# Kernel optimization log

Hardware: AMD Instinct MI355X
Metric: run time of the kernel (lower is better)

The kernel has to match this reference:

```python
import jax, jax.numpy as jnp
import numpy as np

H = 512   # hidden_dim
B = 1024  # batch
D = 256   # history length


def setup_inputs() -> dict:
    key = jax.random.key(0)
    k1, k2, k3, k4, k5, k6 = jax.random.split(key, 6)
    return {
        "h_tilde": jax.random.normal(k1, (B, H), dtype=jnp.float32),
        "c_t": jax.random.normal(k2, (B, H), dtype=jnp.float32),
        "h_history": jax.random.normal(k3, (B, D, H), dtype=jnp.float32),
        # learned parameters (nn.Linear stores weight as [out, in]; y = x @ W.T)
        "Waq": jax.random.normal(k4, (H, 2 * H), dtype=jnp.float32) * (1.0 / np.sqrt(2 * H)),
        "Wah": jax.random.normal(k5, (H, H), dtype=jnp.float32) * (1.0 / np.sqrt(H)),
        "ba": jnp.zeros((H,), dtype=jnp.float32),
        "v_t": jax.random.normal(k6, (H,), dtype=jnp.float32),
    }


def reference(h_tilde, c_t, h_history, Waq, Wah, ba, v_t):
    # q_t = [h_tilde ; c_t] -> [B, 2H]; project to [B, H]
    q_t = jnp.concatenate([h_tilde, c_t], axis=1)
    q_proj = q_t @ Waq.T                         # [B, H]
    h_proj = jnp.einsum('bdh,gh->bdg', h_history, Wah)  # [B, D, H]
    # broadcast add + tanh: the large [B, D, H] intermediate
    score_pre = jnp.tanh(q_proj[:, None, :] + h_proj + ba)
    alpha_unscaled = jnp.einsum('bdh,h->bd', score_pre, v_t)  # [B, D]
    alpha = jax.nn.softmax(alpha_unscaled, axis=1)            # [B, D]
    e_t = jnp.einsum('bd,bdh->bh', alpha, h_history)          # [B, H]
    return (e_t, alpha)
```

## Files before the change

### kernel.cpp

```cpp
#include <hip/hip_runtime.h>
#include <hip/hip_bf16.h>

#define HDIM 512
#define BDIM 1024
#define DDIM 256
#define MTOT (BDIM * DDIM)

typedef _Float16 half8 __attribute__((ext_vector_type(8)));
typedef float f32x4 __attribute__((ext_vector_type(4)));

__device__ __forceinline__ float ftanh(float x) {
    float e = __expf(2.0f * x);
    return 1.0f - 2.0f / (e + 1.0f);
}

__device__ __forceinline__ void gl_lds16(const _Float16* src, _Float16* dst) {
    __builtin_amdgcn_global_load_lds((const __attribute__((address_space(1))) void*)src,
                                     (__attribute__((address_space(3))) void*)dst,
                                     16, 0, 0);
}

__global__ __launch_bounds__(256) void k_convertW(const float* __restrict__ Wah,
                                                  _Float16* __restrict__ W16) {
    int n = blockIdx.x * 256 + threadIdx.x;
    int chunk = n >> 10, r = n & 1023;
    int kb = r >> 6, kp = (r >> 4) & 3, g = r & 15;
    const float* src = Wah + (size_t)(chunk * 16 + g) * 512 + kb * 32 + kp * 8;
    float4 v0 = *(const float4*)src;
    float4 v1 = *(const float4*)(src + 4);
    half8 h;
    h[0] = (_Float16)v0.x; h[1] = (_Float16)v0.y; h[2] = (_Float16)v0.z; h[3] = (_Float16)v0.w;
    h[4] = (_Float16)v1.x; h[5] = (_Float16)v1.y; h[6] = (_Float16)v1.z; h[7] = (_Float16)v1.w;
    *(half8*)&W16[(size_t)n * 8] = h;
}

__global__ __launch_bounds__(256) void k_qproj(const float* __restrict__ h_tilde,
                                               const float* __restrict__ c_t,
                                               const float* __restrict__ Waq,
                                               const float* __restrict__ ba,
                                               float* __restrict__ qb) {
    __shared__ float qs[4][1024];
    int t = threadIdx.x;
    int b0 = blockIdx.x * 4;
    #pragma unroll
    for (int p = 0; p < 4; p++) {
        int f4 = t + p * 256;
        int e = f4 * 4;
        int row = e >> 10, k = e & 1023;
        float4 v;
        if (k < 512) v = *(const float4*)&h_tilde[(b0 + row) * 512 + k];
        else         v = *(const float4*)&c_t[(b0 + row) * 512 + k - 512];
        *(float4*)&qs[row][k] = v;
    }
    __syncthreads();
    int g0 = t, g1 = t + 256;
    float acc0[4] = {0.f, 0.f, 0.f, 0.f};
    float acc1[4] = {0.f, 0.f, 0.f, 0.f};
    const float4* w0p = (const float4*)&Waq[(size_t)g0 * 1024];
    const float4* w1p = (const float4*)&Waq[(size_t)g1 * 1024];
    #pragma unroll 4
    for (int k4 = 0; k4 < 256; k4++) {
        float4 w0 = w0p[k4];
        float4 w1 = w1p[k4];
        #pragma unroll
        for (int bb = 0; bb < 4; bb++) {
            float4 q = *(const float4*)&qs[bb][k4 * 4];
            acc0[bb] += q.x * w0.x + q.y * w0.y + q.z * w0.z + q.w * w0.w;
            acc1[bb] += q.x * w1.x + q.y * w1.y + q.z * w1.z + q.w * w1.w;
        }
    }
    #pragma unroll
    for (int bb = 0; bb < 4; bb++) {
        qb[(b0 + bb) * 512 + g0] = acc0[bb] + ba[g0];
        qb[(b0 + bb) * 512 + g1] = acc1[bb] + ba[g1];
    }
}

__global__ __launch_bounds__(256, 4) void k_logits(const float* __restrict__ hist,
                                                   const float* __restrict__ qb,
                                                   const _Float16* __restrict__ W16,
                                                   const float* __restrict__ v_t,
                                                   float* __restrict__ logits) {
    __shared__ _Float16 Wb[2][8192];
    __shared__ float qbs[512];
    __shared__ float vsh[512];

    int t = threadIdx.x;
    int w = t >> 6, lane = t & 63, l15 = lane & 15, l4 = lane >> 4;
    size_t m_base = (size_t)blockIdx.x * 64;
    int b = blockIdx.x >> 2;

    qbs[t] = qb[b * 512 + t];
    qbs[t + 256] = qb[b * 512 + 256 + t];
    vsh[t] = v_t[t];
    vsh[t + 256] = v_t[256 + t];

    #pragma unroll
    for (int sg = 0; sg < 4; sg++)
        gl_lds16(W16 + ((size_t)(w * 4 + sg) * 64 + lane) * 8,
                 &Wb[0][(w * 4 + sg) * 512]);

    half8 afr[16];
    const float* xb = hist + (m_base + w * 16 + l15) * 512 + l4 * 8;
    #pragma unroll
    for (int kb = 0; kb < 16; kb++) {
        const float* p = xb + kb * 32;
        float4 v0 = *(const float4*)p;
        float4 v1 = *(const float4*)(p + 4);
        half8 h;
        h[0] = (_Float16)v0.x; h[1] = (_Float16)v0.y; h[2] = (_Float16)v0.z; h[3] = (_Float16)v0.w;
        h[4] = (_Float16)v1.x; h[5] = (_Float16)v1.y; h[6] = (_Float16)v1.z; h[7] = (_Float16)v1.w;
        afr[kb] = h;
    }

    float S[4] = {0.f, 0.f, 0.f, 0.f};

    __syncthreads();

    const _Float16* bufbase0 = &Wb[0][lane * 8];
    const _Float16* bufbase1 = &Wb[1][lane * 8];

    for (int c = 0; c < 32; c++) {
        int cur = c & 1;
        if (c < 31) {
            const _Float16* wc = W16 + (size_t)(c + 1) * 8192;
            _Float16* wd = Wb[cur ^ 1];
            #pragma unroll
            for (int sg = 0; sg < 4; sg++)
                gl_lds16(wc + ((size_t)(w * 4 + sg) * 64 + lane) * 8,
                         &wd[(w * 4 + sg) * 512]);
        }
        const _Float16* bufp = cur ? bufbase1 : bufbase0;
        f32x4 tac = (f32x4){0.f, 0.f, 0.f, 0.f};
        __builtin_amdgcn_s_setprio(1);
        #pragma unroll
        for (int kb = 0; kb < 16; kb++) {
            half8 bf = *(const half8*)(bufp + kb * 512);
            tac = __builtin_amdgcn_mfma_f32_16x16x32_f16(afr[kb], bf, tac, 0, 0, 0);
        }
        __builtin_amdgcn_s_setprio(0);
        float qv = qbs[c * 16 + l15];
        float vv = vsh[c * 16 + l15];
        #pragma unroll
        for (int j = 0; j < 4; j++)
            S[j] += ftanh(tac[j] + qv) * vv;
        __syncthreads();
    }

    #pragma unroll
    for (int j = 0; j < 4; j++) {
        float s = S[j];
        s += __shfl_xor(s, 1, 64);
        s += __shfl_xor(s, 2, 64);
        s += __shfl_xor(s, 4, 64);
        s += __shfl_xor(s, 8, 64);
        if (l15 == 0)
            logits[m_base + w * 16 + l4 * 4 + j] = s;
    }
}

__global__ __launch_bounds__(256) void k_softmax_et(const float* __restrict__ hist,
                                                    const float* __restrict__ logits,
                                                    float* __restrict__ out) {
    __shared__ float as_[256];
    __shared__ float wred[4];
    __shared__ float ered[512];
    int b = blockIdx.x, t = threadIdx.x;
    float l = logits[b * 256 + t];
    float m = l;
    m = fmaxf(m, __shfl_xor(m, 1, 64));
    m = fmaxf(m, __shfl_xor(m, 2, 64));
    m = fmaxf(m, __shfl_xor(m, 4, 64));
    m = fmaxf(m, __shfl_xor(m, 8, 64));
    m = fmaxf(m, __shfl_xor(m, 16, 64));
    m = fmaxf(m, __shfl_xor(m, 32, 64));
    if ((t & 63) == 0) wred[t >> 6] = m;
    __syncthreads();
    m = fmaxf(fmaxf(wred[0], wred[1]), fmaxf(wred[2], wred[3]));
    float e = __expf(l - m);
    float s = e;
    s += __shfl_xor(s, 1, 64);
    s += __shfl_xor(s, 2, 64);
    s += __shfl_xor(s, 4, 64);
    s += __shfl_xor(s, 8, 64);
    s += __shfl_xor(s, 16, 64);
    s += __shfl_xor(s, 32, 64);
    __syncthreads();
    if ((t & 63) == 0) wred[t >> 6] = s;
    __syncthreads();
    s = wred[0] + wred[1] + wred[2] + wred[3];
    float a = e / s;
    out[BDIM * HDIM + b * 256 + t] = a;
    as_[t] = a;
    __syncthreads();
    int c4 = (t & 127) * 4;
    int dp = t >> 7;
    float e0 = 0.f, e1 = 0.f, e2 = 0.f, e3 = 0.f;
    const float* hb = hist + (size_t)b * 256 * 512 + c4;
    #pragma unroll 4
    for (int d = dp; d < 256; d += 2) {
        float al = as_[d];
        float4 h = *(const float4*)&hb[(size_t)d * 512];
        e0 += al * h.x; e1 += al * h.y; e2 += al * h.z; e3 += al * h.w;
    }
    if (dp) {
        float4 v; v.x = e0; v.y = e1; v.z = e2; v.w = e3;
        *(float4*)&ered[c4] = v;
    }
    __syncthreads();
    if (!dp) {
        float4 p = *(const float4*)&ered[c4];
        float4 r; r.x = e0 + p.x; r.y = e1 + p.y; r.z = e2 + p.z; r.w = e3 + p.w;
        *(float4*)&out[b * 512 + c4] = r;
    }
}

extern "C" void kernel_launch(void* const* d_in, const int* in_sizes, int n_in,
                              void* d_out, int out_size, void* d_ws, size_t ws_size,
                              hipStream_t stream) {
    const float* h_tilde = (const float*)d_in[0];
    const float* c_t     = (const float*)d_in[1];
    const float* hist    = (const float*)d_in[2];
    const float* Waq     = (const float*)d_in[3];
    const float* Wah     = (const float*)d_in[4];
    const float* ba      = (const float*)d_in[5];
    const float* v_t     = (const float*)d_in[6];
    float* out = (float*)d_out;

    char* ws = (char*)d_ws;
    float*    qb     = (float*)ws;
    _Float16* W16    = (_Float16*)(ws + (2u << 20));
    float*    logits = (float*)(ws + (3u << 20));

    k_convertW<<<128, 256, 0, stream>>>(Wah, W16);
    k_qproj<<<256, 256, 0, stream>>>(h_tilde, c_t, Waq, ba, qb);
    k_logits<<<4096, 256, 0, stream>>>(hist, qb, W16, v_t, logits);
    k_softmax_et<<<1024, 256, 0, stream>>>(hist, logits, out);
}
```

Before: 414.4 us.

## Retile logits GEMM into 128x128 MFMA tiles with fp16 history cache for softmax

Replaces the per-64-row logits kernel with a 128x128 tiled MFMA GEMM that stages both A (history converted to fp16) and B in LDS with double buffering, splitting the N dimension across 4 blocks and writing partial logits. The nb==0 blocks also write an fp16 copy of the history, which the softmax/e_t kernel reads instead of the fp32 tensor, halving that pass's bytes. It merges W conversion and q projection into one prep launch and uses a raw v_rcp in tanh. The cost is 4x reread of the history across N-blocks (likely cache-served), an extra 256MB fp16 write, and reduced precision for e_t.

```diff
diff --git a/kernel.cpp b/kernel.cpp
--- a/kernel.cpp
+++ b/kernel.cpp
@@ -7,11 +7,15 @@
 #define MTOT (BDIM * DDIM)
 
 typedef _Float16 half8 __attribute__((ext_vector_type(8)));
+typedef _Float16 half4_ __attribute__((ext_vector_type(4)));
 typedef float f32x4 __attribute__((ext_vector_type(4)));
 
 __device__ __forceinline__ float ftanh(float x) {
     float e = __expf(2.0f * x);
-    return 1.0f - 2.0f / (e + 1.0f);
+    float d = e + 1.0f;
+    float r;
+    asm("v_rcp_f32 %0, %1" : "=v"(r) : "v"(d));
+    return 1.0f - 2.0f * r;
 }
 
 __device__ __forceinline__ void gl_lds16(const _Float16* src, _Float16* dst) {
@@ -20,153 +24,207 @@
                                      16, 0, 0);
 }
 
-__global__ __launch_bounds__(256) void k_convertW(const float* __restrict__ Wah,
-                                                  _Float16* __restrict__ W16) {
-    int n = blockIdx.x * 256 + threadIdx.x;
-    int chunk = n >> 10, r = n & 1023;
-    int kb = r >> 6, kp = (r >> 4) & 3, g = r & 15;
-    const float* src = Wah + (size_t)(chunk * 16 + g) * 512 + kb * 32 + kp * 8;
-    float4 v0 = *(const float4*)src;
-    float4 v1 = *(const float4*)(src + 4);
-    half8 h;
-    h[0] = (_Float16)v0.x; h[1] = (_Float16)v0.y; h[2] = (_Float16)v0.z; h[3] = (_Float16)v0.w;
-    h[4] = (_Float16)v1.x; h[5] = (_Float16)v1.y; h[6] = (_Float16)v1.z; h[7] = (_Float16)v1.w;
-    *(half8*)&W16[(size_t)n * 8] = h;
-}
-
-__global__ __launch_bounds__(256) void k_qproj(const float* __restrict__ h_tilde,
-                                               const float* __restrict__ c_t,
-                                               const float* __restrict__ Waq,
-                                               const float* __restrict__ ba,
-                                               float* __restrict__ qb) {
-    __shared__ float qs[4][1024];
+__global__ __launch_bounds__(256) void k_prep(const float* __restrict__ h_tilde,
+                                              const float* __restrict__ c_t,
+                                              const float* __restrict__ Waq,
+                                              const float* __restrict__ ba,
+                                              const float* __restrict__ Wah,
+                                              float* __restrict__ qb,
+                                              _Float16* __restrict__ W16) {
+    __shared__ float qs[16][1024];
     int t = threadIdx.x;
-    int b0 = blockIdx.x * 4;
-    #pragma unroll
-    for (int p = 0; p < 4; p++) {
-        int f4 = t + p * 256;
-        int e = f4 * 4;
-        int row = e >> 10, k = e & 1023;
+    if (blockIdx.x >= 256) {
+        int n = (blockIdx.x - 256) * 256 + t;
+        int ch = n >> 9, r = n & 511;
+        int j = r >> 6, l = r & 63;
+        int col = (ch >> 4) * 128 + j * 16 + (l & 15);
+        int k = (ch & 15) * 32 + (l >> 4) * 8;
+        const float* src = Wah + (size_t)col * 512 + k;
+        float4 v0 = *(const float4*)src;
+        float4 v1 = *(const float4*)(src + 4);
+        half8 h;
+        h[0] = (_Float16)v0.x; h[1] = (_Float16)v0.y; h[2] = (_Float16)v0.z; h[3] = (_Float16)v0.w;
+        h[4] = (_Float16)v1.x; h[5] = (_Float16)v1.y; h[6] = (_Float16)v1.z; h[7] = (_Float16)v1.w;
+        *(half8*)&W16[(size_t)n * 8] = h;
+        return;
+    }
+    int bt = blockIdx.x >> 2, gq = blockIdx.x & 3;
+    int b0 = bt * 16;
+    #pragma unroll
+    for (int i = 0; i < 16; i++) {
+        int idx = t + i * 256;
+        int row = idx >> 8, k = (idx & 255) * 4;
         float4 v;
         if (k < 512) v = *(const float4*)&h_tilde[(b0 + row) * 512 + k];
         else         v = *(const float4*)&c_t[(b0 + row) * 512 + k - 512];
         *(float4*)&qs[row][k] = v;
     }
     __syncthreads();
-    int g0 = t, g1 = t + 256;
-    float acc0[4] = {0.f, 0.f, 0.f, 0.f};
-    float acc1[4] = {0.f, 0.f, 0.f, 0.f};
-    const float4* w0p = (const float4*)&Waq[(size_t)g0 * 1024];
-    const float4* w1p = (const float4*)&Waq[(size_t)g1 * 1024];
-    #pragma unroll 4
+    int g = gq * 128 + (t & 127);
+    int bh = t >> 7;
+    float acc[8] = {0.f, 0.f, 0.f, 0.f, 0.f, 0.f, 0.f, 0.f};
+    const float4* wp = (const float4*)&Waq[(size_t)g * 1024];
+    #pragma unroll 2
     for (int k4 = 0; k4 < 256; k4++) {
-        float4 w0 = w0p[k4];
-        float4 w1 = w1p[k4];
-        #pragma unroll
-        for (int bb = 0; bb < 4; bb++) {
-            float4 q = *(const float4*)&qs[bb][k4 * 4];
-            acc0[bb] += q.x * w0.x + q.y * w0.y + q.z * w0.z + q.w * w0.w;
-            acc1[bb] += q.x * w1.x + q.y * w1.y + q.z * w1.z + q.w * w1.w;
-        }
-    }
-    #pragma unroll
-    for (int bb = 0; bb < 4; bb++) {
-        qb[(b0 + bb) * 512 + g0] = acc0[bb] + ba[g0];
-        qb[(b0 + bb) * 512 + g1] = acc1[bb] + ba[g1];
-    }
-}
-
-__global__ __launch_bounds__(256, 4) void k_logits(const float* __restrict__ hist,
-                                                   const float* __restrict__ qb,
-                                                   const _Float16* __restrict__ W16,
-                                                   const float* __restrict__ v_t,
-                                                   float* __restrict__ logits) {
-    __shared__ _Float16 Wb[2][8192];
-    __shared__ float qbs[512];
-    __shared__ float vsh[512];
+        float4 wv = wp[k4];
+        #pragma unroll
+        for (int j = 0; j < 8; j++) {
+            float4 q = *(const float4*)&qs[bh * 8 + j][k4 * 4];
+            acc[j] += q.x * wv.x + q.y * wv.y + q.z * wv.z + q.w * wv.w;
+        }
+    }
+    float bav = ba[g];
+    #pragma unroll
+    for (int j = 0; j < 8; j++)
+        qb[(b0 + bh * 8 + j) * 512 + g] = acc[j] + bav;
+}
+
+template<int STORE16>
+__global__ __launch_bounds__(256, 3) void k_gemm(const float* __restrict__ hist,
+                                                 const float* __restrict__ qb,
+                                                 const _Float16* __restrict__ W16,
+                                                 const float* __restrict__ v_t,
+                                                 float* __restrict__ logitP,
+                                                 _Float16* __restrict__ hist16) {
+    __shared__ _Float16 Ab[2][4096];
+    __shared__ _Float16 Bb[2][4096];
+    __shared__ float qbs[128];
+    __shared__ float vsh[128];
+    __shared__ float red[2][128];
 
     int t = threadIdx.x;
     int w = t >> 6, lane = t & 63, l15 = lane & 15, l4 = lane >> 4;
-    size_t m_base = (size_t)blockIdx.x * 64;
-    int b = blockIdx.x >> 2;
-
-    qbs[t] = qb[b * 512 + t];
-    qbs[t + 256] = qb[b * 512 + 256 + t];
-    vsh[t] = v_t[t];
-    vsh[t + 256] = v_t[256 + t];
-
-    #pragma unroll
-    for (int sg = 0; sg < 4; sg++)
-        gl_lds16(W16 + ((size_t)(w * 4 + sg) * 64 + lane) * 8,
-                 &Wb[0][(w * 4 + sg) * 512]);
-
-    half8 afr[16];
-    const float* xb = hist + (m_base + w * 16 + l15) * 512 + l4 * 8;
-    #pragma unroll
-    for (int kb = 0; kb < 16; kb++) {
-        const float* p = xb + kb * 32;
-        float4 v0 = *(const float4*)p;
-        float4 v1 = *(const float4*)(p + 4);
-        half8 h;
-        h[0] = (_Float16)v0.x; h[1] = (_Float16)v0.y; h[2] = (_Float16)v0.z; h[3] = (_Float16)v0.w;
-        h[4] = (_Float16)v1.x; h[5] = (_Float16)v1.y; h[6] = (_Float16)v1.z; h[7] = (_Float16)v1.w;
-        afr[kb] = h;
-    }
-
-    float S[4] = {0.f, 0.f, 0.f, 0.f};
-
-    __syncthreads();
-
-    const _Float16* bufbase0 = &Wb[0][lane * 8];
-    const _Float16* bufbase1 = &Wb[1][lane * 8];
-
-    for (int c = 0; c < 32; c++) {
-        int cur = c & 1;
-        if (c < 31) {
-            const _Float16* wc = W16 + (size_t)(c + 1) * 8192;
-            _Float16* wd = Wb[cur ^ 1];
+    int bx = blockIdx.x;
+    int xslot = bx & 7, nb = (bx >> 3) & 3;
+    int mt = (bx >> 5) * 8 + xslot;
+    size_t m_base = (size_t)mt * 128;
+    int b = mt >> 1;
+    int wr = w >> 1, wc = w & 1;
+
+    if (t < 128) {
+        qbs[t] = qb[b * 512 + nb * 128 + t];
+        vsh[t] = v_t[nb * 128 + t];
+    }
+
+    const _Float16* wch = W16 + (size_t)nb * 16 * 4096;
+
+    const float* asrc = hist + (m_base + (t >> 1)) * 512 + (t & 1) * 16;
+    const int ga0 = ((t >> 5) * 64 + (t & 1) * 32 + ((t >> 1) & 15)) * 8;
+    const int ga1 = ga0 + 128;
+    _Float16* h16dst = hist16 + (m_base + (t >> 1)) * 512 + (t & 1) * 16;
+
+    #pragma unroll
+    for (int sg = 0; sg < 2; sg++)
+        gl_lds16(wch + ((size_t)(w * 2 + sg) * 64 + lane) * 8,
+                 &Bb[0][(w * 2 + sg) * 512]);
+    float4 xa0 = *(const float4*)(asrc);
+    float4 xa1 = *(const float4*)(asrc + 4);
+    float4 xa2 = *(const float4*)(asrc + 8);
+    float4 xa3 = *(const float4*)(asrc + 12);
+    {
+        half8 h0, h1;
+        h0[0] = (_Float16)xa0.x; h0[1] = (_Float16)xa0.y; h0[2] = (_Float16)xa0.z; h0[3] = (_Float16)xa0.w;
+        h0[4] = (_Float16)xa1.x; h0[5] = (_Float16)xa1.y; h0[6] = (_Float16)xa1.z; h0[7] = (_Float16)xa1.w;
+        h1[0] = (_Float16)xa2.x; h1[1] = (_Float16)xa2.y; h1[2] = (_Float16)xa2.z; h1[3] = (_Float16)xa2.w;
+        h1[4] = (_Float16)xa3.x; h1[5] = (_Float16)xa3.y; h1[6] = (_Float16)xa3.z; h1[7] = (_Float16)xa3.w;
+        *(half8*)&Ab[0][ga0] = h0;
+        *(half8*)&Ab[0][ga1] = h1;
+        if (STORE16 && nb == 0) {
+            *(half8*)(h16dst) = h0;
+            *(half8*)(h16dst + 8) = h1;
+        }
+    }
+    __syncthreads();
+
+    f32x4 acc[4][4];
+    #pragma unroll
+    for (int i = 0; i < 4; i++)
+        #pragma unroll
+        for (int j = 0; j < 4; j++)
+            acc[i][j] = (f32x4){0.f, 0.f, 0.f, 0.f};
+
+    for (int s = 0; s < 16; s++) {
+        int cur = s & 1;
+        if (s < 15) {
+            const _Float16* wc2 = wch + (size_t)(s + 1) * 4096;
+            _Float16* bd = Bb[cur ^ 1];
             #pragma unroll
-            for (int sg = 0; sg < 4; sg++)
-                gl_lds16(wc + ((size_t)(w * 4 + sg) * 64 + lane) * 8,
-                         &wd[(w * 4 + sg) * 512]);
-        }
-        const _Float16* bufp = cur ? bufbase1 : bufbase0;
-        f32x4 tac = (f32x4){0.f, 0.f, 0.f, 0.f};
+            for (int sg = 0; sg < 2; sg++)
+                gl_lds16(wc2 + ((size_t)(w * 2 + sg) * 64 + lane) * 8,
+                         &bd[(w * 2 + sg) * 512]);
+            const float* pa = asrc + (s + 1) * 32;
+            xa0 = *(const float4*)(pa);
+            xa1 = *(const float4*)(pa + 4);
+            xa2 = *(const float4*)(pa + 8);
+            xa3 = *(const float4*)(pa + 12);
+        }
+        const _Float16* ap = Ab[cur];
+        const _Float16* bp = Bb[cur];
+        half8 afv[4], bfv[4];
+        #pragma unroll
+        for (int i = 0; i < 4; i++)
+            afv[i] = *(const half8*)&ap[((wr * 4 + i) * 64 + lane) * 8];
+        #pragma unroll
+        for (int j = 0; j < 4; j++)
+            bfv[j] = *(const half8*)&bp[((wc * 4 + j) * 64 + lane) * 8];
         __builtin_amdgcn_s_setprio(1);
         #pragma unroll
-        for (int kb = 0; kb < 16; kb++) {
-            half8 bf = *(const half8*)(bufp + kb * 512);
-            tac = __builtin_amdgcn_mfma_f32_16x16x32_f16(afr[kb], bf, tac, 0, 0, 0);
-        }
+        for (int i = 0; i < 4; i++)
+            #pragma unroll
+            for (int j = 0; j < 4; j++)
+                acc[i][j] = __builtin_amdgcn_mfma_f32_16x16x32_f16(afv[i], bfv[j], acc[i][j], 0, 0, 0);
         __builtin_amdgcn_s_setprio(0);
-        float qv = qbs[c * 16 + l15];
-        float vv = vsh[c * 16 + l15];
-        #pragma unroll
-        for (int j = 0; j < 4; j++)
-            S[j] += ftanh(tac[j] + qv) * vv;
+        if (s < 15) {
+            half8 h0, h1;
+            h0[0] = (_Float16)xa0.x; h0[1] = (_Float16)xa0.y; h0[2] = (_Float16)xa0.z; h0[3] = (_Float16)xa0.w;
+            h0[4] = (_Float16)xa1.x; h0[5] = (_Float16)xa1.y; h0[6] = (_Float16)xa1.z; h0[7] = (_Float16)xa1.w;
+            h1[0] = (_Float16)xa2.x; h1[1] = (_Float16)xa2.y; h1[2] = (_Float16)xa2.z; h1[3] = (_Float16)xa2.w;
+            h1[4] = (_Float16)xa3.x; h1[5] = (_Float16)xa3.y; h1[6] = (_Float16)xa3.z; h1[7] = (_Float16)xa3.w;
+            _Float16* ad = Ab[cur ^ 1];
+            *(half8*)&ad[ga0] = h0;
+            *(half8*)&ad[ga1] = h1;
+            if (STORE16 && nb == 0) {
+                *(half8*)(h16dst + (s + 1) * 32) = h0;
+                *(half8*)(h16dst + (s + 1) * 32 + 8) = h1;
+            }
+        }
         __syncthreads();
     }
 
     #pragma unroll
-    for (int j = 0; j < 4; j++) {
-        float s = S[j];
-        s += __shfl_xor(s, 1, 64);
-        s += __shfl_xor(s, 2, 64);
-        s += __shfl_xor(s, 4, 64);
-        s += __shfl_xor(s, 8, 64);
-        if (l15 == 0)
-            logits[m_base + w * 16 + l4 * 4 + j] = s;
-    }
-}
-
+    for (int i = 0; i < 4; i++) {
+        #pragma unroll
+        for (int r = 0; r < 4; r++) {
+            float s_ = 0.0f;
+            #pragma unroll
+            for (int j = 0; j < 4; j++) {
+                int col = wc * 64 + j * 16 + l15;
+                s_ += ftanh(acc[i][j][r] + qbs[col]) * vsh[col];
+            }
+            s_ += __shfl_xor(s_, 1, 64);
+            s_ += __shfl_xor(s_, 2, 64);
+            s_ += __shfl_xor(s_, 4, 64);
+            s_ += __shfl_xor(s_, 8, 64);
+            if (l15 == 0)
+                red[wc][wr * 64 + i * 16 + l4 * 4 + r] = s_;
+        }
+    }
+    __syncthreads();
+    if (t < 128)
+        logitP[(size_t)nb * MTOT + m_base + t] = red[0][t] + red[1][t];
+}
+
+template<int USE16>
 __global__ __launch_bounds__(256) void k_softmax_et(const float* __restrict__ hist,
-                                                    const float* __restrict__ logits,
+                                                    const _Float16* __restrict__ h16,
+                                                    const float* __restrict__ logitP,
                                                     float* __restrict__ out) {
     __shared__ float as_[256];
     __shared__ float wred[4];
     __shared__ float ered[512];
     int b = blockIdx.x, t = threadIdx.x;
-    float l = logits[b * 256 + t];
+    int m0i = b * 256 + t;
+    float l = logitP[m0i] + logitP[MTOT + m0i] + logitP[2 * MTOT + m0i] + logitP[3 * MTOT + m0i];
     float m = l;
     m = fmaxf(m, __shfl_xor(m, 1, 64));
     m = fmaxf(m, __shfl_xor(m, 2, 64));
@@ -196,12 +254,23 @@
     int c4 = (t & 127) * 4;
     int dp = t >> 7;
     float e0 = 0.f, e1 = 0.f, e2 = 0.f, e3 = 0.f;
-    const float* hb = hist + (size_t)b * 256 * 512 + c4;
-    #pragma unroll 4
-    for (int d = dp; d < 256; d += 2) {
-        float al = as_[d];
-        float4 h = *(const float4*)&hb[(size_t)d * 512];
-        e0 += al * h.x; e1 += al * h.y; e2 += al * h.z; e3 += al * h.w;
+    if (USE16) {
+        const _Float16* hb = h16 + (size_t)b * 256 * 512 + c4;
+        #pragma unroll 4
+        for (int d = dp; d < 256; d += 2) {
+            float al = as_[d];
+            half4_ h = *(const half4_*)&hb[(size_t)d * 512];
+            e0 += al * (float)h[0]; e1 += al * (float)h[1];
+            e2 += al * (float)h[2]; e3 += al * (float)h[3];
+        }
+    } else {
+        const float* hb = hist + (size_t)b * 256 * 512 + c4;
+        #pragma unroll 4
+        for (int d = dp; d < 256; d += 2) {
+            float al = as_[d];
+            float4 h = *(const float4*)&hb[(size_t)d * 512];
+            e0 += al * h.x; e1 += al * h.y; e2 += al * h.z; e3 += al * h.w;
+        }
     }
     if (dp) {
         float4 v; v.x = e0; v.y = e1; v.z = e2; v.w = e3;
@@ -230,10 +299,16 @@
     char* ws = (char*)d_ws;
     float*    qb     = (float*)ws;
     _Float16* W16    = (_Float16*)(ws + (2u << 20));
-    float*    logits = (float*)(ws + (3u << 20));
-
-    k_convertW<<<128, 256, 0, stream>>>(Wah, W16);
-    k_qproj<<<256, 256, 0, stream>>>(h_tilde, c_t, Waq, ba, qb);
-    k_logits<<<4096, 256, 0, stream>>>(hist, qb, W16, v_t, logits);
-    k_softmax_et<<<1024, 256, 0, stream>>>(hist, logits, out);
-}
+    float*    logitP = (float*)(ws + (3u << 20));
+    _Float16* hist16 = (_Float16*)(ws + (8u << 20));
+    bool use16 = ws_size >= (size_t)(8u << 20) + (size_t)MTOT * 512 * 2;
+
+    k_prep<<<384, 256, 0, stream>>>(h_tilde, c_t, Waq, ba, Wah, qb, W16);
+    if (use16) {
+        k_gemm<1><<<8192, 256, 0, stream>>>(hist, qb, W16, v_t, logitP, hist16);
+        k_softmax_et<1><<<1024, 256, 0, stream>>>(hist, hist16, logitP, out);
+    } else {
+        k_gemm<0><<<8192, 256, 0, stream>>>(hist, qb, W16, v_t, logitP, hist16);
+        k_softmax_et<0><<<1024, 256, 0, stream>>>(hist, hist16, logitP, out);
+    }
+}
```

Measured after the change: 443.6 us. 7.0% more time.
